# Kernel optimization log

Hardware: AMD Instinct MI355X
Metric: run time of the kernel (lower is better)

Reference implementation:

```python
import jax, jax.numpy as jnp
import numpy as np
from jax import lax

EDGES = [(11,12),(11,23),(12,24),(23,24),(23,25),(25,27),(24,26),(26,28),(11,13),(13,15),(12,14),(14,16)]
J = 33

def _build_neighbors():
    nb = [[j] for j in range(J)]
    for a, b in EDGES:
        nb[a].append(b); nb[b].append(a)
    K = max(len(n) for n in nb)
    idx = np.zeros((J, K), np.int32)
    msk = np.zeros((J, K), np.float32)
    for j, n in enumerate(nb):
        idx[j, :len(n)] = n; msk[j, :len(n)] = 1.0
    return jnp.asarray(idx), jnp.asarray(msk)

NBR_IDX, NBR_MASK = _build_neighbors()
BN_EPS = 1e-5

def conv(x, w, b):
    y = lax.conv_general_dilated(x, w, (1, 1), 'SAME', dimension_numbers=('NCHW', 'OIHW', 'NCHW'))
    return y + b[None, :, None, None]

def bn(x, g, b):
    # eval-mode BatchNorm with running_mean=0, running_var=1
    s = g / jnp.sqrt(1.0 + BN_EPS)
    return x * s[None, :, None, None] + b[None, :, None, None]

def maxpool2(x):
    return lax.reduce_window(x, -jnp.inf, lax.max, (1, 1, 2, 2), (1, 1, 2, 2), 'VALID')

def deconv2x2(x, w, b):
    # ConvTranspose2d(k=2, s=2): w is [Cin, Cout, 2, 2]
    y = jnp.einsum('bcij,codk->boidjk', x, w)
    B, O, H, _, W, _ = y.shape
    return y.reshape(B, O, 2 * H, 2 * W) + b[None, :, None, None]

def forward(x, conv1_w, conv1_b, bn1_g, bn1_b, conv2_w, conv2_b, bn2_g, bn2_b,
            conv3_w, conv3_b, bn3_g, bn3_b, conv4_w, conv4_b, bn4_g, bn4_b,
            dc1_w, dc1_b, dc2_w, dc2_b, head_w, head_b, proj_w, proj_b,
            msg_w, msg_b, gru_w_ih, gru_w_hh, gru_b_ih, gru_b_hh,
            refine_w, refine_b, vis_w1, vis_b1, vis_w2, vis_b2):
    relu = jax.nn.relu
    h = bn(relu(conv(x, conv1_w, conv1_b)), bn1_g, bn1_b)
    h = bn(relu(conv(h, conv2_w, conv2_b)), bn2_g, bn2_b)
    h = maxpool2(h)
    h = bn(relu(conv(h, conv3_w, conv3_b)), bn3_g, bn3_b)
    h = maxpool2(h)
    enc = bn(relu(conv(h, conv4_w, conv4_b)), bn4_g, bn4_b)  # [B,256,H/4,W/4]
    f = relu(deconv2x2(enc, dc1_w, dc1_b))
    feat_map = relu(deconv2x2(f, dc2_w, dc2_b))  # [B,64,H,W]
    init_hm = jax.nn.sigmoid(conv(feat_map, head_w, head_b))  # [B,J,H,W]
    B, Jn, H, W = init_hm.shape
    sm = jax.nn.softmax(init_hm.reshape(B, Jn, H * W) / 0.1, axis=-1).reshape(B, Jn, H, W)
    w_idx = jnp.linspace(0.0, 1.0, W)
    h_idx = jnp.linspace(0.0, 1.0, H)
    pred_x = (sm.sum(-2) * w_idx).sum(-1)  # [B,J] in [0,1]
    pred_y = (sm.sum(-1) * h_idx).sum(-1)
    # grid_sample bilinear, align_corners=True: grid=(2p-1) -> pixel coord p*(dim-1)
    ix = pred_x * (W - 1)
    iy = pred_y * (H - 1)
    x0 = jnp.clip(jnp.floor(ix), 0, W - 1)
    y0 = jnp.clip(jnp.floor(iy), 0, H - 1)
    wx = ix - x0
    wy = iy - y0
    x0i = x0.astype(jnp.int32); x1i = jnp.clip(x0i + 1, 0, W - 1)
    y0i = y0.astype(jnp.int32); y1i = jnp.clip(y0i + 1, 0, H - 1)
    fm = feat_map.transpose(0, 2, 3, 1)  # [B,H,W,C]
    bidx = jnp.arange(B)[:, None]
    v00 = fm[bidx, y0i, x0i]; v01 = fm[bidx, y0i, x1i]
    v10 = fm[bidx, y1i, x0i]; v11 = fm[bidx, y1i, x1i]
    wx = wx[..., None]; wy = wy[..., None]
    joint = (v00 * (1 - wx) * (1 - wy) + v01 * wx * (1 - wy)
             + v10 * (1 - wx) * wy + v11 * wx * wy)  # [B,J,64]
    joint_feats = joint @ proj_w.T + proj_b
    # SkeletonGNN (all joints read original joint_feats -> fully parallel)
    gathered = joint_feats[:, NBR_IDX, :]  # [B,J,K,D]
    lin = gathered @ msg_w.T + msg_b
    m = NBR_MASK[None, :, :, None]
    msgs = (lin * m).sum(2) / NBR_MASK.sum(1)[None, :, None]  # [B,J,D]
    gi = msgs @ gru_w_ih.T + gru_b_ih
    gh = joint_feats @ gru_w_hh.T + gru_b_hh
    D = joint_feats.shape[-1]
    ir, iz, inn = gi[..., :D], gi[..., D:2 * D], gi[..., 2 * D:]
    hr, hz, hn = gh[..., :D], gh[..., D:2 * D], gh[..., 2 * D:]
    r = jax.nn.sigmoid(ir + hr)
    z = jax.nn.sigmoid(iz + hz)
    n = jnp.tanh(inn + r * hn)
    refined_feats = (1 - z) * n + z * joint_feats
    refined_bias = refined_feats.mean(-1)[:, :, None, None]
    refined_hm = jax.nn.sigmoid(conv(init_hm, refine_w, refine_b) + refined_bias)
    # visibility head: adaptive avg pool to 4x4 (enc HW divisible by 4), eval dropout = identity
    eB, eC, eH, eW = enc.shape
    p = enc.reshape(eB, eC, 4, eH // 4, 4, eW // 4).mean((3, 5))  # [B,256,4,4]
    v = jax.nn.relu(p.reshape(eB, -1) @ vis_w1.T + vis_b1)
    vis_pred = jax.nn.sigmoid(v @ vis_w2.T + vis_b2)
    return refined_hm, vis_pred

def setup_inputs() -> dict:
    key = jax.random.key(0)
    ks = iter(jax.random.split(key, 64))
    def w(shape, s=0.05):
        return (jax.random.normal(next(ks), shape, dtype=jnp.float32) * s)
    inp = {
        'x': jax.random.normal(next(ks), (16, 3, 256, 256), dtype=jnp.float32),
        'conv1_w': w((32, 3, 3, 3)), 'conv1_b': w((32,)), 'bn1_g': jnp.ones((32,)), 'bn1_b': jnp.zeros((32,)),
        'conv2_w': w((64, 32, 3, 3)), 'conv2_b': w((64,)), 'bn2_g': jnp.ones((64,)), 'bn2_b': jnp.zeros((64,)),
        'conv3_w': w((128, 64, 3, 3)), 'conv3_b': w((128,)), 'bn3_g': jnp.ones((128,)), 'bn3_b': jnp.zeros((128,)),
        'conv4_w': w((256, 128, 3, 3)), 'conv4_b': w((256,)), 'bn4_g': jnp.ones((256,)), 'bn4_b': jnp.zeros((256,)),
        'dc1_w': w((256, 128, 2, 2)), 'dc1_b': w((128,)),
        'dc2_w': w((128, 64, 2, 2)), 'dc2_b': w((64,)),
        'head_w': w((33, 64, 1, 1)), 'head_b': w((33,)),
        'proj_w': w((64, 64)), 'proj_b': w((64,)),
        'msg_w': w((64, 64)), 'msg_b': w((64,)),
        'gru_w_ih': w((192, 64)), 'gru_w_hh': w((192, 64)),
        'gru_b_ih': w((192,)), 'gru_b_hh': w((192,)),
        'refine_w': w((33, 33, 3, 3)), 'refine_b': w((33,)),
        'vis_w1': w((256, 256 * 16)), 'vis_b1': w((256,)),
        'vis_w2': w((33, 256)), 'vis_b2': w((33,)),
    }
    return inp

def reference(x, conv1_w, conv1_b, bn1_g, bn1_b, conv2_w, conv2_b, bn2_g, bn2_b,
              conv3_w, conv3_b, bn3_g, bn3_b, conv4_w, conv4_b, bn4_g, bn4_b,
              dc1_w, dc1_b, dc2_w, dc2_b, head_w, head_b, proj_w, proj_b,
              msg_w, msg_b, gru_w_ih, gru_w_hh, gru_b_ih, gru_b_hh,
              refine_w, refine_b, vis_w1, vis_b1, vis_w2, vis_b2):
    return forward(x, conv1_w, conv1_b, bn1_g, bn1_b, conv2_w, conv2_b, bn2_g, bn2_b,
                   conv3_w, conv3_b, bn3_g, bn3_b, conv4_w, conv4_b, bn4_g, bn4_b,
                   dc1_w, dc1_b, dc2_w, dc2_b, head_w, head_b, proj_w, proj_b,
                   msg_w, msg_b, gru_w_ih, gru_w_hh, gru_b_ih, gru_b_hh,
                   refine_w, refine_b, vis_w1, vis_b1, vis_w2, vis_b2)
```

## Files before the change

### kernel.cpp

```cpp
#include <hip/hip_runtime.h>
#include <hip/hip_bf16.h>
#include <math.h>

#define BN_RS 0.99999500003749977f

typedef __attribute__((ext_vector_type(8))) __bf16 bf16x8;
typedef __attribute__((ext_vector_type(4))) float f32x4;

union U16 { uint4 u; bf16x8 v; __hip_bfloat16 h[8]; };
union U8  { uint2 u; __hip_bfloat16 h[4]; };

__device__ __forceinline__ float sigf(float v) { return 1.0f / (1.0f + expf(-v)); }

__global__ __launch_bounds__(256)
void repack_conv_w_k(const float* __restrict__ w, __hip_bfloat16* __restrict__ wb,
                     int taps, int Co, int Ci, int CoT, int Kp)
{
    int i = blockIdx.x * 256 + threadIdx.x;
    int tot = taps * CoT * Kp;
    if (i >= tot) return;
    int k = i % Kp, n = (i / Kp) % CoT, t = i / (Kp * CoT);
    float v = (n < Co && k < Ci) ? w[((long)n * Ci + k) * taps + t] : 0.0f;
    wb[i] = __float2bfloat16(v);
}
__global__ __launch_bounds__(256)
void repack_conv_w_ilv_k(const float* __restrict__ w, __hip_bfloat16* __restrict__ wb,
                         int taps, int Co, int Ci, int CoT, int Kp)
{
    int i = blockIdx.x * 256 + threadIdx.x;
    int tot = taps * CoT * Kp;
    if (i >= tot) return;
    int k = i % Kp, n = (i / Kp) % CoT, t = i / (Kp * CoT);
    int grp = n >> 6, r = n & 63;
    int c = (grp << 6) + (r & 15) * 4 + (r >> 4);
    float v = (c < Co && k < Ci) ? w[((long)c * Ci + k) * taps + t] : 0.0f;
    wb[i] = __float2bfloat16(v);
}
__global__ __launch_bounds__(256)
void repack_deconv_w_ilv_k(const float* __restrict__ w, __hip_bfloat16* __restrict__ wb,
                           int Co, int Ci)
{
    int i = blockIdx.x * 256 + threadIdx.x;
    int tot = 4 * Co * Ci;
    if (i >= tot) return;
    int k = i % Ci, n = (i / Ci) % Co, q = i / (Ci * Co);
    int grp = n >> 6, r = n & 63;
    int c = (grp << 6) + (r & 15) * 4 + (r >> 4);
    wb[i] = __float2bfloat16(w[((long)k * Co + c) * 4 + q]);
}

__global__ __launch_bounds__(256)
void zero_halo_k(__hip_bfloat16* __restrict__ buf, int H, int W, int C, int B)
{
    const int P = W + 2;
    const long per = (long)(2 * P + 2 * H) * C;
    long idx = (long)blockIdx.x * 256 + threadIdx.x;
    if (idx >= per * B) return;
    int b = (int)(idx / per);
    long r = idx % per;
    long off;
    if (r < (long)2 * P * C) {
        int row = (r >= (long)P * C) ? (H + 1) : 0;
        long r2 = r % ((long)P * C);
        off = (((long)b * (H + 2) + row) * P) * C + r2;
    } else {
        long r2 = r - (long)2 * P * C;
        int row = 1 + (int)(r2 / (2 * C));
        int side = (int)((r2 / C) & 1);
        int ch = (int)(r2 % C);
        off = (((long)b * (H + 2) + row) * P + (side ? (W + 1) : 0)) * C + ch;
    }
    buf[off] = __float2bfloat16(0.0f);
}

__global__ __launch_bounds__(256)
void conv1_k(const float* __restrict__ x, const float* __restrict__ w,
             const float* __restrict__ cb, const float* __restrict__ g,
             const float* __restrict__ bb, __hip_bfloat16* __restrict__ out)
{
    __shared__ float sw[216];
    const int tid = threadIdx.x;
    const int b = blockIdx.z >> 2, cg = blockIdx.z & 3, co0 = cg * 8;
    for (int i = tid; i < 216; i += 256) {
        int t = i % 9, co = (i / 9) % 8, ci = i / 72;
        sw[i] = w[((co0 + co) * 3 + ci) * 9 + t];
    }
    __syncthreads();
    const int tx = tid & 15, ty = tid >> 4;
    const int y = blockIdx.y * 16 + ty;
    const int xs = blockIdx.x * 64 + tx;
    float acc[4][8];
#pragma unroll
    for (int p = 0; p < 4; ++p)
#pragma unroll
        for (int c = 0; c < 8; ++c) acc[p][c] = 0.0f;
    for (int ci = 0; ci < 3; ++ci) {
        const float* plane = x + ((long)b * 3 + ci) * 65536;
#pragma unroll
        for (int t = 0; t < 9; ++t) {
            const int dy = t / 3 - 1, dx = t % 3 - 1;
            const int yy = y + dy;
            if ((unsigned)yy < 256u) {
                const float* row = plane + yy * 256;
                float wsr[8];
#pragma unroll
                for (int c = 0; c < 8; ++c) wsr[c] = sw[ci * 72 + c * 9 + t];
#pragma unroll
                for (int p = 0; p < 4; ++p) {
                    const int xx = xs + p * 16 + dx;
                    const float v = ((unsigned)xx < 256u) ? row[xx] : 0.0f;
#pragma unroll
                    for (int c = 0; c < 8; ++c) acc[p][c] = fmaf(v, wsr[c], acc[p][c]);
                }
            }
        }
    }
#pragma unroll
    for (int p = 0; p < 4; ++p) {
        U16 o;
#pragma unroll
        for (int c = 0; c < 8; ++c) {
            const int cc = co0 + c;
            float v = fmaxf(acc[p][c] + cb[cc], 0.0f) * (g[cc] * BN_RS) + bb[cc];
            o.h[c] = __float2bfloat16(v);
        }
        *(uint4*)(void*)(out + ((long)b * 2130048L + ((long)y * 258 + xs + p * 16) * 32) + co0) = o.u;
    }
}

template<int MI>
__global__ __launch_bounds__(256)
void mfma_conv_k(const __hip_bfloat16* __restrict__ in,
                 const __hip_bfloat16* __restrict__ wb,
                 const float* __restrict__ cbias,
                 const float* __restrict__ bng, const float* __restrict__ bnb,
                 __hip_bfloat16* __restrict__ out_bf,
                 int H, int W, int Cin, int PIT, long bstride, long obstride, int OPIT,
                 int CoutT, int CG, int S)
{
    const int tid = threadIdx.x;
    const int wid = tid >> 6, lane = tid & 63;
    const int ln = lane & 15, kg = lane >> 4;
    const int nx = gridDim.x;
    const int bx = (blockIdx.x & 7) * (nx >> 3) + (blockIdx.x >> 3);
    const int u = bx * 4 + wid;
    const int y = u / S, x0 = (u % S) * (MI * 16);
    const int b = blockIdx.z / CG, cg = blockIdx.z % CG;
    const int co0 = cg * 64;
    const int KC = Cin >> 5;

    f32x4 acc[MI][4];
#pragma unroll
    for (int i = 0; i < MI; ++i)
#pragma unroll
        for (int j = 0; j < 4; ++j) acc[i][j] = f32x4{0.f, 0.f, 0.f, 0.f};

    for (int kc = 0; kc < KC; ++kc) {
        const int kofs = kc * 32 + kg * 8;
#pragma unroll
        for (int t = 0; t < 9; ++t) {
            const int dy = t / 3 - 1, dx = t % 3 - 1;
            bf16x8 wfr[4];
#pragma unroll
            for (int ni = 0; ni < 4; ++ni)
                wfr[ni] = *(const bf16x8*)(const void*)(wb + ((long)t * CoutT + co0 + ni * 16 + ln) * Cin + kofs);
            U16 av[MI];
            const long rowb = (long)b * bstride + (long)(y + dy) * PIT * Cin + kofs;
#pragma unroll
            for (int mi = 0; mi < MI; ++mi)
                av[mi].u = *(const uint4*)(const void*)(in + rowb + (long)(x0 + mi * 16 + ln + dx) * Cin);
#pragma unroll
            for (int mi = 0; mi < MI; ++mi)
#pragma unroll
                for (int ni = 0; ni < 4; ++ni)
                    acc[mi][ni] = __builtin_amdgcn_mfma_f32_16x16x32_bf16(av[mi].v, wfr[ni], acc[mi][ni], 0, 0, 0);
        }
    }
#pragma unroll
    for (int mi = 0; mi < MI; ++mi) {
#pragma unroll
        for (int r = 0; r < 4; ++r) {
            const int px = x0 + mi * 16 + kg * 4 + r;
            const long pb = (long)b * obstride + ((long)y * OPIT + px) * CoutT + co0;
            U8 o;
#pragma unroll
            for (int ni = 0; ni < 4; ++ni) {
                const int c = co0 + ln * 4 + ni;
                float v = acc[mi][ni][r] + cbias[c];
                v = fmaxf(v, 0.0f) * (bng[c] * BN_RS) + bnb[c];
                o.h[ni] = __float2bfloat16(v);
            }
            *(uint2*)(void*)(out_bf + pb + ln * 4) = o.u;
        }
    }
}

__global__ __launch_bounds__(256)
void mfma_deconv_k(const __hip_bfloat16* __restrict__ in,
                   const __hip_bfloat16* __restrict__ wb,
                   const float* __restrict__ bias,
                   __hip_bfloat16* __restrict__ out,
                   int H, int W, int Cin, int CoutT, int CG, int S)
{
    const int tid = threadIdx.x;
    const int wid = tid >> 6, lane = tid & 63;
    const int ln = lane & 15, kg = lane >> 4;
    const int nx = gridDim.x;
    const int bx = (blockIdx.x & 7) * (nx >> 3) + (blockIdx.x >> 3);
    const int u = bx * 4 + wid;
    const int y = u / S, x0 = (u % S) * 32;
    const int b = blockIdx.z / CG, cg = blockIdx.z % CG;
    const int co0 = cg * 64;
    const int KC = Cin >> 5;
    const long inb = (long)b * H * W * Cin;
    const int W2 = W * 2;
    const long ob = (long)b * 4 * H * W * CoutT;

    for (int q = 0; q < 4; ++q) {
        const int dy = q >> 1, dx = q & 1;
        f32x4 acc[2][4];
#pragma unroll
        for (int i = 0; i < 2; ++i)
#pragma unroll
            for (int j = 0; j < 4; ++j) acc[i][j] = f32x4{0.f, 0.f, 0.f, 0.f};
        for (int kc = 0; kc < KC; ++kc) {
            const int kofs = kc * 32 + kg * 8;
            bf16x8 wfr[4];
            U16 av[2];
#pragma unroll
            for (int ni = 0; ni < 4; ++ni)
                wfr[ni] = *(const bf16x8*)(const void*)(wb + ((long)q * CoutT + co0 + ni * 16 + ln) * Cin + kofs);
#pragma unroll
            for (int mi = 0; mi < 2; ++mi)
                av[mi].u = *(const uint4*)(const void*)(in + inb + ((long)y * W + x0 + mi * 16 + ln) * Cin + kofs);
#pragma unroll
            for (int mi = 0; mi < 2; ++mi)
#pragma unroll
                for (int ni = 0; ni < 4; ++ni)
                    acc[mi][ni] = __builtin_amdgcn_mfma_f32_16x16x32_bf16(av[mi].v, wfr[ni], acc[mi][ni], 0, 0, 0);
        }
#pragma unroll
        for (int mi = 0; mi < 2; ++mi) {
#pragma unroll
            for (int r = 0; r < 4; ++r) {
                const int xl = x0 + mi * 16 + kg * 4 + r;
                const long pb = ob + ((long)(2 * y + dy) * W2 + 2 * xl + dx) * CoutT + co0;
                U8 o;
#pragma unroll
                for (int ni = 0; ni < 4; ++ni) {
                    const int c = co0 + ln * 4 + ni;
                    float v = fmaxf(acc[mi][ni][r] + bias[c], 0.0f);
                    o.h[ni] = __float2bfloat16(v);
                }
                *(uint2*)(void*)(out + pb + ln * 4) = o.u;
            }
        }
    }
}

template<int MODE>
__global__ __launch_bounds__(256)
void mfma_convT_k(const __hip_bfloat16* __restrict__ in,
                  const __hip_bfloat16* __restrict__ wb,
                  const float* __restrict__ cbias, const float* __restrict__ ebias,
                  __hip_bfloat16* __restrict__ out_bf, float* __restrict__ out_f32,
                  int H, int W, int Cin, int PIT, long bstride, long obstride, int OPIT,
                  int CoutT, int S)
{
    extern __shared__ float ltr[];
    const int tid = threadIdx.x;
    const int wid = tid >> 6, lane = tid & 63;
    const int ln = lane & 15, kg = lane >> 4;
    const int nx = gridDim.x;
    const int bx = (blockIdx.x & 7) * (nx >> 3) + (blockIdx.x >> 3);
    const int u = bx * 4 + wid;
    const int y = u / S, x0 = (u % S) * 32;
    const int b = blockIdx.z;
    const int KC = Cin >> 5;

    f32x4 acc[2][3];
#pragma unroll
    for (int i = 0; i < 2; ++i)
#pragma unroll
        for (int j = 0; j < 3; ++j) acc[i][j] = f32x4{0.f, 0.f, 0.f, 0.f};

    constexpr int NT = (MODE == 1) ? 1 : 9;
    for (int kc = 0; kc < KC; ++kc) {
        const int kofs = kc * 32 + kg * 8;
#pragma unroll
        for (int t = 0; t < NT; ++t) {
            const int dy = (MODE == 1) ? 0 : (t / 3 - 1);
            const int dx = (MODE == 1) ? 0 : (t % 3 - 1);
            bf16x8 wfr[3];
#pragma unroll
            for (int ni = 0; ni < 3; ++ni)
                wfr[ni] = *(const bf16x8*)(const void*)(wb + ((long)t * CoutT + ni * 16 + ln) * Cin + kofs);
            U16 av[2];
            const long rowb = (long)b * bstride + (long)(y + dy) * PIT * Cin + kofs;
#pragma unroll
            for (int mi = 0; mi < 2; ++mi)
                av[mi].u = *(const uint4*)(const void*)(in + rowb + (long)(x0 + mi * 16 + ln + dx) * Cin);
#pragma unroll
            for (int mi = 0; mi < 2; ++mi)
#pragma unroll
                for (int ni = 0; ni < 3; ++ni)
                    acc[mi][ni] = __builtin_amdgcn_mfma_f32_16x16x32_bf16(av[mi].v, wfr[ni], acc[mi][ni], 0, 0, 0);
        }
    }

    float* wt = ltr + wid * (48 * 35);
#pragma unroll
    for (int mi = 0; mi < 2; ++mi) {
#pragma unroll
        for (int r = 0; r < 4; ++r) {
            const int pxl = mi * 16 + kg * 4 + r;
            const int px = x0 + pxl;
#pragma unroll
            for (int ni = 0; ni < 3; ++ni) {
                const int c = ni * 16 + ln;
                float v = acc[mi][ni][r];
                if constexpr (MODE == 1) {
                    v = sigf(v + ((c < 33) ? cbias[c] : 0.0f));
                    out_bf[(long)b * obstride + ((long)y * OPIT + px) * CoutT + c] =
                        (c < 33) ? __float2bfloat16(v) : __float2bfloat16(0.0f);
                } else {
                    float eb = (c < 33) ? (cbias[c] + ebias[b * 33 + c]) : 0.0f;
                    v = sigf(v + eb);
                }
                wt[c * 35 + pxl] = v;
            }
        }
    }
    if (lane < 32) {
        const long o32 = ((long)b * 33) * H * W + (long)y * W + x0 + lane;
        for (int c = 0; c < 33; ++c)
            out_f32[o32 + (long)c * H * W] = wt[c * 35 + lane];
    }
}

__global__ __launch_bounds__(256)
void maxpool_bf_k(const __hip_bfloat16* __restrict__ in, __hip_bfloat16* __restrict__ out,
                  int Ho, int Wo, int C, long total, int OPIT, long obstride)
{
    long idx = (long)blockIdx.x * 256 + threadIdx.x;
    if (idx >= total) return;
    const int ng = C >> 3;
    const int cg = (int)(idx % ng);
    long pix = idx / ng;
    const int xo = (int)(pix % Wo); pix /= Wo;
    const int yo = (int)(pix % Ho);
    const int b = (int)(pix / Ho);
    const int Wi = Wo * 2;
    const __hip_bfloat16* p = in + (((long)b * 2 * Ho + 2 * yo) * Wi + 2 * xo) * C + cg * 8;
    U16 a0, a1, a2, a3, o;
    a0.u = *(const uint4*)(const void*)p;
    a1.u = *(const uint4*)(const void*)(p + C);
    a2.u = *(const uint4*)(const void*)(p + (long)Wi * C);
    a3.u = *(const uint4*)(const void*)(p + (long)Wi * C + C);
#pragma unroll
    for (int j = 0; j < 8; ++j) {
        float m = fmaxf(fmaxf(__bfloat162float(a0.h[j]), __bfloat162float(a1.h[j])),
                        fmaxf(__bfloat162float(a2.h[j]), __bfloat162float(a3.h[j])));
        o.h[j] = __float2bfloat16(m);
    }
    *(uint4*)(void*)(out + (long)b * obstride + ((long)yo * OPIT + xo) * C + cg * 8) = o.u;
}

__global__ __launch_bounds__(256)
void softargmax_k(const float* __restrict__ hm, float* __restrict__ coords)
{
    __shared__ float r0[256], r1[256], r2[256];
    const int bj = blockIdx.x;
    const int tid = threadIdx.x;
    const float* row = hm + (long)bj * 65536;
    float m = -1e30f;
    for (int i = tid; i < 65536; i += 256) m = fmaxf(m, row[i]);
    r0[tid] = m;
    __syncthreads();
    for (int s = 128; s > 0; s >>= 1) {
        if (tid < s) r0[tid] = fmaxf(r0[tid], r0[tid + s]);
        __syncthreads();
    }
    const float mx = r0[0];
    __syncthreads();
    float s = 0.0f, sx = 0.0f, sy = 0.0f;
    for (int i = tid; i < 65536; i += 256) {
        float e = expf((row[i] - mx) * 10.0f);
        s += e;
        sx += e * (float)(i & 255);
        sy += e * (float)(i >> 8);
    }
    r0[tid] = s; r1[tid] = sx; r2[tid] = sy;
    __syncthreads();
    for (int st = 128; st > 0; st >>= 1) {
        if (tid < st) { r0[tid] += r0[tid + st]; r1[tid] += r1[tid + st]; r2[tid] += r2[tid + st]; }
        __syncthreads();
    }
    if (tid == 0) {
        coords[2 * bj] = r1[0] / r0[0];
        coords[2 * bj + 1] = r2[0] / r0[0];
    }
}

__global__ __launch_bounds__(64)
void joint_bf_k(const __hip_bfloat16* __restrict__ fm, const float* __restrict__ coords,
                const float* __restrict__ pw, const float* __restrict__ pb,
                float* __restrict__ jf)
{
    __shared__ float sj[64];
    const int bj = blockIdx.x, b = bj / 33;
    const int tid = threadIdx.x;
    float ix = coords[2 * bj], iy = coords[2 * bj + 1];
    float x0f = fminf(fmaxf(floorf(ix), 0.0f), 255.0f);
    float y0f = fminf(fmaxf(floorf(iy), 0.0f), 255.0f);
    float wx = ix - x0f, wy = iy - y0f;
    int x0 = (int)x0f, y0 = (int)y0f;
    int x1 = min(x0 + 1, 255), y1 = min(y0 + 1, 255);
    const __hip_bfloat16* base = fm + (long)b * 65536 * 64 + tid;
    float v00 = __bfloat162float(base[((long)y0 * 256 + x0) * 64]);
    float v01 = __bfloat162float(base[((long)y0 * 256 + x1) * 64]);
    float v10 = __bfloat162float(base[((long)y1 * 256 + x0) * 64]);
    float v11 = __bfloat162float(base[((long)y1 * 256 + x1) * 64]);
    sj[tid] = v00 * (1 - wx) * (1 - wy) + v01 * wx * (1 - wy)
            + v10 * (1 - wx) * wy + v11 * wx * wy;
    __syncthreads();
    float a = pb[tid];
    for (int k = 0; k < 64; ++k) a = fmaf(sj[k], pw[tid * 64 + k], a);
    jf[(long)bj * 64 + tid] = a;
}

__device__ const int d_nbr[33][4] = {
    {0,0,0,0},{1,0,0,0},{2,0,0,0},{3,0,0,0},{4,0,0,0},{5,0,0,0},{6,0,0,0},{7,0,0,0},
    {8,0,0,0},{9,0,0,0},{10,0,0,0},
    {11,12,23,13},{12,11,24,14},{13,11,15,0},{14,12,16,0},{15,13,0,0},{16,14,0,0},
    {17,0,0,0},{18,0,0,0},{19,0,0,0},{20,0,0,0},{21,0,0,0},{22,0,0,0},
    {23,11,24,25},{24,12,23,26},{25,23,27,0},{26,24,28,0},{27,25,0,0},{28,26,0,0},
    {29,0,0,0},{30,0,0,0},{31,0,0,0},{32,0,0,0}};
__device__ const int d_cnt[33] = {1,1,1,1,1,1,1,1,1,1,1,4,4,3,3,2,2,1,1,1,1,1,1,4,4,3,3,2,2,1,1,1,1};

__global__ __launch_bounds__(192)
void gru_k(const float* __restrict__ jf, const float* __restrict__ mw, const float* __restrict__ mb,
           const float* __restrict__ wih, const float* __restrict__ whh,
           const float* __restrict__ bih, const float* __restrict__ bhh,
           float* __restrict__ rbias)
{
    __shared__ float s_mjf[64], s_jf[64], s_msg[64], s_gi[192], s_gh[192], s_ref[64];
    const int bj = blockIdx.x;
    const int b = bj / 33, j = bj % 33;
    const int tid = threadIdx.x;
    if (tid < 64) {
        int cnt = d_cnt[j];
        float s = 0.0f;
        for (int n = 0; n < 4; ++n)
            if (n < cnt) s += jf[((long)b * 33 + d_nbr[j][n]) * 64 + tid];
        s_mjf[tid] = s / (float)cnt;
        s_jf[tid] = jf[(long)bj * 64 + tid];
    }
    __syncthreads();
    if (tid < 64) {
        float a = mb[tid];
        for (int k = 0; k < 64; ++k) a = fmaf(mw[tid * 64 + k], s_mjf[k], a);
        s_msg[tid] = a;
    }
    __syncthreads();
    {
        float a = bih[tid], c = bhh[tid];
        for (int k = 0; k < 64; ++k) {
            a = fmaf(wih[tid * 64 + k], s_msg[k], a);
            c = fmaf(whh[tid * 64 + k], s_jf[k], c);
        }
        s_gi[tid] = a; s_gh[tid] = c;
    }
    __syncthreads();
    if (tid < 64) {
        float r = sigf(s_gi[tid] + s_gh[tid]);
        float z = sigf(s_gi[64 + tid] + s_gh[64 + tid]);
        float n = tanhf(s_gi[128 + tid] + r * s_gh[128 + tid]);
        s_ref[tid] = (1.0f - z) * n + z * s_jf[tid];
    }
    __syncthreads();
    if (tid == 0) {
        float s = 0.0f;
        for (int k = 0; k < 64; ++k) s += s_ref[k];
        rbias[bj] = s * (1.0f / 64.0f);
    }
}

__global__ __launch_bounds__(256)
void vispool_bf_k(const __hip_bfloat16* __restrict__ enc, float* __restrict__ p)
{
    int idx = blockIdx.x * 256 + threadIdx.x;
    int v = idx & 3, uu = (idx >> 2) & 3, c = (idx >> 4) & 255, b = idx >> 12;
    const __hip_bfloat16* base = enc + (long)b * 64 * 64 * 256 + c;
    float s = 0.0f;
    for (int a = 0; a < 16; ++a)
#pragma unroll
        for (int d = 0; d < 16; ++d)
            s += __bfloat162float(base[((long)(uu * 16 + a) * 64 + (v * 16 + d)) * 256]);
    p[idx] = s * (1.0f / 256.0f);
}

__global__ __launch_bounds__(256)
void visfc1_k(const float* __restrict__ p, const float* __restrict__ w1,
              const float* __restrict__ b1, float* __restrict__ v1)
{
    __shared__ float s_p[4096];
    const int b = blockIdx.x, tid = threadIdx.x;
    for (int i = tid; i < 4096; i += 256) s_p[i] = p[b * 4096 + i];
    __syncthreads();
    float a = b1[tid];
    const float* wr = w1 + (long)tid * 4096;
    for (int k = 0; k < 4096; ++k) a = fmaf(wr[k], s_p[k], a);
    v1[b * 256 + tid] = fmaxf(a, 0.0f);
}

__global__ __launch_bounds__(64)
void visfc2_k(const float* __restrict__ v1, const float* __restrict__ w2,
              const float* __restrict__ b2, float* __restrict__ out)
{
    const int b = blockIdx.x, t = threadIdx.x;
    if (t < 33) {
        float a = b2[t];
        for (int k = 0; k < 256; ++k) a = fmaf(w2[t * 256 + k], v1[b * 256 + k], a);
        out[b * 33 + t] = sigf(a);
    }
}

extern "C" void kernel_launch(void* const* d_in, const int* in_sizes, int n_in,
                              void* d_out, int out_size, void* d_ws, size_t ws_size,
                              hipStream_t stream)
{
    const float* x   = (const float*)d_in[0];
    const float* c1w = (const float*)d_in[1];  const float* c1b = (const float*)d_in[2];
    const float* b1g = (const float*)d_in[3];  const float* b1b = (const float*)d_in[4];
    const float* c2w = (const float*)d_in[5];  const float* c2b = (const float*)d_in[6];
    const float* b2g = (const float*)d_in[7];  const float* b2b = (const float*)d_in[8];
    const float* c3w = (const float*)d_in[9];  const float* c3b = (const float*)d_in[10];
    const float* b3g = (const float*)d_in[11]; const float* b3b = (const float*)d_in[12];
    const float* c4w = (const float*)d_in[13]; const float* c4b = (const float*)d_in[14];
    const float* b4g = (const float*)d_in[15]; const float* b4b = (const float*)d_in[16];
    const float* d1w = (const float*)d_in[17]; const float* d1b = (const float*)d_in[18];
    const float* d2w = (const float*)d_in[19]; const float* d2b = (const float*)d_in[20];
    const float* hw  = (const float*)d_in[21]; const float* hb  = (const float*)d_in[22];
    const float* pw  = (const float*)d_in[23]; const float* pb  = (const float*)d_in[24];
    const float* mw  = (const float*)d_in[25]; const float* mb  = (const float*)d_in[26];
    const float* wih = (const float*)d_in[27]; const float* whh = (const float*)d_in[28];
    const float* bih = (const float*)d_in[29]; const float* bhh = (const float*)d_in[30];
    const float* rw  = (const float*)d_in[31]; const float* rb  = (const float*)d_in[32];
    const float* v1w = (const float*)d_in[33]; const float* v1b = (const float*)d_in[34];
    const float* v2w = (const float*)d_in[35]; const float* v2b = (const float*)d_in[36];

    char* ws = (char*)d_ws;
    __hip_bfloat16* ENC  = (__hip_bfloat16*)(ws + 0L);
    __hip_bfloat16* R1   = (__hip_bfloat16*)(ws + 33554432L);
    __hip_bfloat16* R2   = (__hip_bfloat16*)(ws + 167772160L);
    char*           R3c  = ws + 304095232L;
    char* SM = ws + 442507264L;

    __hip_bfloat16* H1B = R1;                 __hip_bfloat16* H1I = R1 + 8288;
    __hip_bfloat16* P1B = R1;                 __hip_bfloat16* P1I = R1 + 8384;
    __hip_bfloat16* FEAT = R1;
    __hip_bfloat16* H3  = R2;
    __hip_bfloat16* F   = R2;
    __hip_bfloat16* HDB = R2;                 __hip_bfloat16* HDI = R2 + 16576;
    __hip_bfloat16* P2B = (__hip_bfloat16*)R3c; __hip_bfloat16* P2I = P2B + 8576;
    float*          INITHM = (float*)R3c;

    __hip_bfloat16* W2B = (__hip_bfloat16*)(SM + 0);
    __hip_bfloat16* W3B = (__hip_bfloat16*)(SM + 36864);
    __hip_bfloat16* W4B = (__hip_bfloat16*)(SM + 184320);
    __hip_bfloat16* WRB = (__hip_bfloat16*)(SM + 774144);
    __hip_bfloat16* WHB = (__hip_bfloat16*)(SM + 847872);
    __hip_bfloat16* WD1 = (__hip_bfloat16*)(SM + 856064);
    __hip_bfloat16* WD2 = (__hip_bfloat16*)(SM + 1118208);
    float* CO = (float*)(SM + 1183744);
    float* JF = (float*)(SM + 1187968);
    float* RB = (float*)(SM + 1323136);
    float* P  = (float*)(SM + 1325248);
    float* V1 = (float*)(SM + 1587392);

    float* out_hm  = (float*)d_out;
    float* out_vis = out_hm + 34603008L;
    __hip_bfloat16* H2 = (__hip_bfloat16*)d_out;

    repack_conv_w_ilv_k<<<(9*64*32 + 255)/256, 256, 0, stream>>>(c2w, W2B, 9, 64, 32, 64, 32);
    repack_conv_w_ilv_k<<<(9*128*64 + 255)/256, 256, 0, stream>>>(c3w, W3B, 9, 128, 64, 128, 64);
    repack_conv_w_ilv_k<<<(9*256*128 + 255)/256, 256, 0, stream>>>(c4w, W4B, 9, 256, 128, 256, 128);
    repack_conv_w_k<<<(9*64*64 + 255)/256, 256, 0, stream>>>(rw, WRB, 9, 33, 33, 64, 64);
    repack_conv_w_k<<<(1*64*64 + 255)/256, 256, 0, stream>>>(hw, WHB, 1, 33, 64, 64, 64);
    repack_deconv_w_ilv_k<<<(4*128*256 + 255)/256, 256, 0, stream>>>(d1w, WD1, 128, 256);
    repack_deconv_w_ilv_k<<<(4*64*128 + 255)/256, 256, 0, stream>>>(d2w, WD2, 64, 128);

    zero_halo_k<<<(526336 + 255)/256, 256, 0, stream>>>(H1B, 256, 256, 32, 16);
    zero_halo_k<<<(532480 + 255)/256, 256, 0, stream>>>(P2B, 64, 64, 128, 16);

    conv1_k<<<dim3(4, 16, 64), 256, 0, stream>>>(x, c1w, c1b, b1g, b1b, H1I);
    mfma_conv_k<2><<<dim3(512, 1, 16), 256, 0, stream>>>(
        H1I, W2B, c2b, b2g, b2b, H2,
        256, 256, 32, 258, 2130048L, 4194304L, 256, 64, 1, 8);
    zero_halo_k<<<(528384 + 255)/256, 256, 0, stream>>>(P1B, 128, 128, 64, 16);
    maxpool_bf_k<<<8192, 256, 0, stream>>>(H2, P1I, 128, 128, 64, 2097152L, 130, 1081600L);
    mfma_conv_k<2><<<dim3(128, 1, 32), 256, 0, stream>>>(
        P1I, W3B, c3b, b3g, b3b, H3,
        128, 128, 64, 130, 1081600L, 2097152L, 128, 128, 2, 4);
    maxpool_bf_k<<<4096, 256, 0, stream>>>(H3, P2I, 64, 64, 128, 1048576L, 66, 557568L);
    mfma_conv_k<2><<<dim3(32, 1, 64), 256, 0, stream>>>(
        P2I, W4B, c4b, b4g, b4b, ENC,
        64, 64, 128, 66, 557568L, 1048576L, 64, 256, 4, 2);
    mfma_deconv_k<<<dim3(32, 1, 32), 256, 0, stream>>>(
        ENC, WD1, d1b, F, 64, 64, 256, 128, 2, 2);
    mfma_deconv_k<<<dim3(128, 1, 16), 256, 0, stream>>>(
        F, WD2, d2b, FEAT, 128, 128, 128, 64, 1, 4);
    zero_halo_k<<<(1052672 + 255)/256, 256, 0, stream>>>(HDB, 256, 256, 64, 16);
    mfma_convT_k<1><<<dim3(512, 1, 16), 256, 26880, stream>>>(
        FEAT, WHB, hb, nullptr, HDI, INITHM,
        256, 256, 64, 256, 4194304L, 4260096L, 258, 64, 8);
    softargmax_k<<<528, 256, 0, stream>>>(INITHM, CO);
    joint_bf_k<<<528, 64, 0, stream>>>(FEAT, CO, pw, pb, JF);
    gru_k<<<528, 192, 0, stream>>>(JF, mw, mb, wih, whh, bih, bhh, RB);
    mfma_convT_k<2><<<dim3(512, 1, 16), 256, 26880, stream>>>(
        HDI, WRB, rb, RB, nullptr, out_hm,
        256, 256, 64, 258, 4260096L, 0L, 0, 64, 8);
    vispool_bf_k<<<256, 256, 0, stream>>>(ENC, P);
    visfc1_k<<<16, 256, 0, stream>>>(P, v1w, v1b, V1);
    visfc2_k<<<16, 64, 0, stream>>>(V1, v2w, v2b, out_vis);
}
```

Baseline: 1.731 ms.

## Drop fp32 init heatmap, softargmax from bf16 NHWC, coalesce refine stores

The head conv no longer writes a separate fp32 NCHW heatmap. It writes only the bf16 padded NHWC buffer with packed 4-channel stores, using interleaved weights. Softargmax now reads that bf16 NHWC buffer directly, handling 8 joints per block on a 16x5 grid instead of 528 blocks. The refine kernel's output is staged in shared memory and written cooperatively as 128-pixel contiguous runs per channel with rotated channel order, replacing 32-lane strided stores. The intent is to cut memory traffic and improve store coalescing. The tradeoffs are softargmax precision from bf16 inputs and far fewer softargmax blocks, which limits parallelism.

```diff
diff --git a/kernel.cpp b/kernel.cpp
--- a/kernel.cpp
+++ b/kernel.cpp
@@ -258,25 +258,76 @@
     }
 }
 
-template<int MODE>
-__global__ __launch_bounds__(256)
-void mfma_convT_k(const __hip_bfloat16* __restrict__ in,
-                  const __hip_bfloat16* __restrict__ wb,
-                  const float* __restrict__ cbias, const float* __restrict__ ebias,
-                  __hip_bfloat16* __restrict__ out_bf, float* __restrict__ out_f32,
-                  int H, int W, int Cin, int PIT, long bstride, long obstride, int OPIT,
-                  int CoutT, int S)
-{
-    extern __shared__ float ltr[];
+__global__ __launch_bounds__(256)
+void mfma_head_k(const __hip_bfloat16* __restrict__ in,
+                 const __hip_bfloat16* __restrict__ wb,
+                 const float* __restrict__ hb,
+                 __hip_bfloat16* __restrict__ out)
+{
     const int tid = threadIdx.x;
     const int wid = tid >> 6, lane = tid & 63;
     const int ln = lane & 15, kg = lane >> 4;
     const int nx = gridDim.x;
     const int bx = (blockIdx.x & 7) * (nx >> 3) + (blockIdx.x >> 3);
     const int u = bx * 4 + wid;
-    const int y = u / S, x0 = (u % S) * 32;
+    const int y = u >> 3, x0 = (u & 7) * 32;
     const int b = blockIdx.z;
-    const int KC = Cin >> 5;
+
+    f32x4 acc[2][4];
+#pragma unroll
+    for (int i = 0; i < 2; ++i)
+#pragma unroll
+        for (int j = 0; j < 4; ++j) acc[i][j] = f32x4{0.f, 0.f, 0.f, 0.f};
+
+    for (int kc = 0; kc < 2; ++kc) {
+        const int kofs = kc * 32 + kg * 8;
+        bf16x8 wfr[4];
+#pragma unroll
+        for (int ni = 0; ni < 4; ++ni)
+            wfr[ni] = *(const bf16x8*)(const void*)(wb + ((long)(ni * 16 + ln)) * 64 + kofs);
+        U16 av[2];
+#pragma unroll
+        for (int mi = 0; mi < 2; ++mi)
+            av[mi].u = *(const uint4*)(const void*)(in + (long)b * 4194304L + ((long)y * 256 + x0 + mi * 16 + ln) * 64 + kofs);
+#pragma unroll
+        for (int mi = 0; mi < 2; ++mi)
+#pragma unroll
+            for (int ni = 0; ni < 4; ++ni)
+                acc[mi][ni] = __builtin_amdgcn_mfma_f32_16x16x32_bf16(av[mi].v, wfr[ni], acc[mi][ni], 0, 0, 0);
+    }
+#pragma unroll
+    for (int mi = 0; mi < 2; ++mi) {
+#pragma unroll
+        for (int r = 0; r < 4; ++r) {
+            const int px = x0 + mi * 16 + kg * 4 + r;
+            const long pb = (long)b * 4260096L + ((long)y * 258 + px) * 64;
+            U8 o;
+#pragma unroll
+            for (int ni = 0; ni < 4; ++ni) {
+                const int c = ln * 4 + ni;
+                float v = (c < 33) ? sigf(acc[mi][ni][r] + hb[c]) : 0.0f;
+                o.h[ni] = __float2bfloat16(v);
+            }
+            *(uint2*)(void*)(out + pb + ln * 4) = o.u;
+        }
+    }
+}
+
+__global__ __launch_bounds__(256)
+void mfma_refine_k(const __hip_bfloat16* __restrict__ in,
+                   const __hip_bfloat16* __restrict__ wb,
+                   const float* __restrict__ cbias, const float* __restrict__ ebias,
+                   float* __restrict__ out_f32)
+{
+    extern __shared__ float ltr[];
+    const int tid = threadIdx.x;
+    const int wid = tid >> 6, lane = tid & 63;
+    const int ln = lane & 15, kg = lane >> 4;
+    const int nx = gridDim.x;
+    const int bx = (blockIdx.x & 7) * (nx >> 3) + (blockIdx.x >> 3);
+    const int u = bx * 4 + wid;
+    const int y = u >> 3, x0 = (u & 7) * 32;
+    const int b = blockIdx.z;
 
     f32x4 acc[2][3];
 #pragma unroll
@@ -284,22 +335,20 @@
 #pragma unroll
         for (int j = 0; j < 3; ++j) acc[i][j] = f32x4{0.f, 0.f, 0.f, 0.f};
 
-    constexpr int NT = (MODE == 1) ? 1 : 9;
-    for (int kc = 0; kc < KC; ++kc) {
+    for (int kc = 0; kc < 2; ++kc) {
         const int kofs = kc * 32 + kg * 8;
 #pragma unroll
-        for (int t = 0; t < NT; ++t) {
-            const int dy = (MODE == 1) ? 0 : (t / 3 - 1);
-            const int dx = (MODE == 1) ? 0 : (t % 3 - 1);
+        for (int t = 0; t < 9; ++t) {
+            const int dy = t / 3 - 1, dx = t % 3 - 1;
             bf16x8 wfr[3];
 #pragma unroll
             for (int ni = 0; ni < 3; ++ni)
-                wfr[ni] = *(const bf16x8*)(const void*)(wb + ((long)t * CoutT + ni * 16 + ln) * Cin + kofs);
+                wfr[ni] = *(const bf16x8*)(const void*)(wb + ((long)t * 64 + ni * 16 + ln) * 64 + kofs);
             U16 av[2];
-            const long rowb = (long)b * bstride + (long)(y + dy) * PIT * Cin + kofs;
+            const long rowb = (long)b * 4260096L + (long)(y + dy) * 258 * 64 + kofs;
 #pragma unroll
             for (int mi = 0; mi < 2; ++mi)
-                av[mi].u = *(const uint4*)(const void*)(in + rowb + (long)(x0 + mi * 16 + ln + dx) * Cin);
+                av[mi].u = *(const uint4*)(const void*)(in + rowb + (long)(x0 + mi * 16 + ln + dx) * 64);
 #pragma unroll
             for (int mi = 0; mi < 2; ++mi)
 #pragma unroll
@@ -308,33 +357,29 @@
         }
     }
 
-    float* wt = ltr + wid * (48 * 35);
+    float* wt = ltr + wid * 1680;
 #pragma unroll
     for (int mi = 0; mi < 2; ++mi) {
 #pragma unroll
         for (int r = 0; r < 4; ++r) {
             const int pxl = mi * 16 + kg * 4 + r;
-            const int px = x0 + pxl;
 #pragma unroll
             for (int ni = 0; ni < 3; ++ni) {
                 const int c = ni * 16 + ln;
-                float v = acc[mi][ni][r];
-                if constexpr (MODE == 1) {
-                    v = sigf(v + ((c < 33) ? cbias[c] : 0.0f));
-                    out_bf[(long)b * obstride + ((long)y * OPIT + px) * CoutT + c] =
-                        (c < 33) ? __float2bfloat16(v) : __float2bfloat16(0.0f);
-                } else {
-                    float eb = (c < 33) ? (cbias[c] + ebias[b * 33 + c]) : 0.0f;
-                    v = sigf(v + eb);
-                }
-                wt[c * 35 + pxl] = v;
+                float eb = (c < 33) ? (cbias[c] + ebias[b * 33 + c]) : 0.0f;
+                wt[c * 35 + pxl] = sigf(acc[mi][ni][r] + eb);
             }
         }
     }
-    if (lane < 32) {
-        const long o32 = ((long)b * 33) * H * W + (long)y * W + x0 + lane;
-        for (int c = 0; c < 33; ++c)
-            out_f32[o32 + (long)c * H * W] = wt[c * 35 + lane];
+    __syncthreads();
+    const int yb = (bx * 4) >> 3;
+    const int xb = ((bx * 4) & 7) * 32;
+    const int coff = bx % 33;
+    for (int i = tid; i < 4224; i += 256) {
+        int cl = i >> 7, p = i & 127;
+        int c = cl + coff; if (c >= 33) c -= 33;
+        float v = ltr[(p >> 5) * 1680 + c * 35 + (p & 31)];
+        out_f32[((long)b * 33 + c) * 65536L + (long)yb * 256 + xb + p] = v;
     }
 }
 
@@ -367,38 +412,68 @@
 }
 
 __global__ __launch_bounds__(256)
-void softargmax_k(const float* __restrict__ hm, float* __restrict__ coords)
-{
-    __shared__ float r0[256], r1[256], r2[256];
-    const int bj = blockIdx.x;
-    const int tid = threadIdx.x;
-    const float* row = hm + (long)bj * 65536;
-    float m = -1e30f;
-    for (int i = tid; i < 65536; i += 256) m = fmaxf(m, row[i]);
-    r0[tid] = m;
+void softargmax_nhwc_k(const __hip_bfloat16* __restrict__ hd, float* __restrict__ coords)
+{
+    __shared__ float sm[8][256];
+    __shared__ float fin[8][4];
+    const int b = blockIdx.x, jg = blockIdx.y;
+    const int tid = threadIdx.x;
+    const __hip_bfloat16* base = hd + (long)b * 4260096L + jg * 8;
+    float m[8];
+#pragma unroll
+    for (int c = 0; c < 8; ++c) m[c] = -1e30f;
+    for (int i = tid; i < 65536; i += 256) {
+        int y = i >> 8, x = i & 255;
+        U16 v; v.u = *(const uint4*)(const void*)(base + ((long)y * 258 + x) * 64);
+#pragma unroll
+        for (int c = 0; c < 8; ++c) m[c] = fmaxf(m[c], __bfloat162float(v.h[c]));
+    }
+#pragma unroll
+    for (int c = 0; c < 8; ++c) sm[c][tid] = m[c];
     __syncthreads();
     for (int s = 128; s > 0; s >>= 1) {
-        if (tid < s) r0[tid] = fmaxf(r0[tid], r0[tid + s]);
+        if (tid < s)
+#pragma unroll
+            for (int c = 0; c < 8; ++c) sm[c][tid] = fmaxf(sm[c][tid], sm[c][tid + s]);
         __syncthreads();
     }
-    const float mx = r0[0];
-    __syncthreads();
-    float s = 0.0f, sx = 0.0f, sy = 0.0f;
+    if (tid < 8) fin[tid][0] = sm[tid][0];
+    __syncthreads();
+#pragma unroll
+    for (int c = 0; c < 8; ++c) m[c] = fin[c][0];
+    float s8[8], sx8[8], sy8[8];
+#pragma unroll
+    for (int c = 0; c < 8; ++c) { s8[c] = 0.f; sx8[c] = 0.f; sy8[c] = 0.f; }
     for (int i = tid; i < 65536; i += 256) {
-        float e = expf((row[i] - mx) * 10.0f);
-        s += e;
-        sx += e * (float)(i & 255);
-        sy += e * (float)(i >> 8);
-    }
-    r0[tid] = s; r1[tid] = sx; r2[tid] = sy;
-    __syncthreads();
-    for (int st = 128; st > 0; st >>= 1) {
-        if (tid < st) { r0[tid] += r0[tid + st]; r1[tid] += r1[tid + st]; r2[tid] += r2[tid + st]; }
+        int y = i >> 8, x = i & 255;
+        U16 v; v.u = *(const uint4*)(const void*)(base + ((long)y * 258 + x) * 64);
+#pragma unroll
+        for (int c = 0; c < 8; ++c) {
+            float e = expf((__bfloat162float(v.h[c]) - m[c]) * 10.0f);
+            s8[c] += e; sx8[c] += e * (float)x; sy8[c] += e * (float)y;
+        }
+    }
+    for (int which = 0; which < 3; ++which) {
         __syncthreads();
-    }
-    if (tid == 0) {
-        coords[2 * bj] = r1[0] / r0[0];
-        coords[2 * bj + 1] = r2[0] / r0[0];
+#pragma unroll
+        for (int c = 0; c < 8; ++c)
+            sm[c][tid] = (which == 0) ? s8[c] : (which == 1) ? sx8[c] : sy8[c];
+        __syncthreads();
+        for (int s = 128; s > 0; s >>= 1) {
+            if (tid < s)
+#pragma unroll
+                for (int c = 0; c < 8; ++c) sm[c][tid] += sm[c][tid + s];
+            __syncthreads();
+        }
+        if (tid < 8) fin[tid][1 + which] = sm[tid][0];
+    }
+    __syncthreads();
+    if (tid < 8) {
+        int j = jg * 8 + tid;
+        if (j < 33) {
+            coords[2 * (b * 33 + j)]     = fin[tid][2] / fin[tid][1];
+            coords[2 * (b * 33 + j) + 1] = fin[tid][3] / fin[tid][1];
+        }
     }
 }
 
@@ -564,7 +639,6 @@
     __hip_bfloat16* F   = R2;
     __hip_bfloat16* HDB = R2;                 __hip_bfloat16* HDI = R2 + 16576;
     __hip_bfloat16* P2B = (__hip_bfloat16*)R3c; __hip_bfloat16* P2I = P2B + 8576;
-    float*          INITHM = (float*)R3c;
 
     __hip_bfloat16* W2B = (__hip_bfloat16*)(SM + 0);
     __hip_bfloat16* W3B = (__hip_bfloat16*)(SM + 36864);
@@ -587,7 +661,7 @@
     repack_conv_w_ilv_k<<<(9*128*64 + 255)/256, 256, 0, stream>>>(c3w, W3B, 9, 128, 64, 128, 64);
     repack_conv_w_ilv_k<<<(9*256*128 + 255)/256, 256, 0, stream>>>(c4w, W4B, 9, 256, 128, 256, 128);
     repack_conv_w_k<<<(9*64*64 + 255)/256, 256, 0, stream>>>(rw, WRB, 9, 33, 33, 64, 64);
-    repack_conv_w_k<<<(1*64*64 + 255)/256, 256, 0, stream>>>(hw, WHB, 1, 33, 64, 64, 64);
+    repack_conv_w_ilv_k<<<(1*64*64 + 255)/256, 256, 0, stream>>>(hw, WHB, 1, 33, 64, 64, 64);
     repack_deconv_w_ilv_k<<<(4*128*256 + 255)/256, 256, 0, stream>>>(d1w, WD1, 128, 256);
     repack_deconv_w_ilv_k<<<(4*64*128 + 255)/256, 256, 0, stream>>>(d2w, WD2, 64, 128);
 
@@ -612,15 +686,12 @@
     mfma_deconv_k<<<dim3(128, 1, 16), 256, 0, stream>>>(
         F, WD2, d2b, FEAT, 128, 128, 128, 64, 1, 4);
     zero_halo_k<<<(1052672 + 255)/256, 256, 0, stream>>>(HDB, 256, 256, 64, 16);
-    mfma_convT_k<1><<<dim3(512, 1, 16), 256, 26880, stream>>>(
-        FEAT, WHB, hb, nullptr, HDI, INITHM,
-        256, 256, 64, 256, 4194304L, 4260096L, 258, 64, 8);
-    softargmax_k<<<528, 256, 0, stream>>>(INITHM, CO);
+    mfma_head_k<<<dim3(512, 1, 16), 256, 0, stream>>>(FEAT, WHB, hb, HDI);
+    softargmax_nhwc_k<<<dim3(16, 5), 256, 0, stream>>>(HDI, CO);
     joint_bf_k<<<528, 64, 0, stream>>>(FEAT, CO, pw, pb, JF);
     gru_k<<<528, 192, 0, stream>>>(JF, mw, mb, wih, whh, bih, bhh, RB);
-    mfma_convT_k<2><<<dim3(512, 1, 16), 256, 26880, stream>>>(
-        HDI, WRB, rb, RB, nullptr, out_hm,
-        256, 256, 64, 258, 4260096L, 0L, 0, 64, 8);
+    mfma_refine_k<<<dim3(512, 1, 16), 256, 26880, stream>>>(
+        HDI, WRB, rb, RB, out_hm);
     vispool_bf_k<<<256, 256, 0, stream>>>(ENC, P);
     visfc1_k<<<16, 256, 0, stream>>>(P, v1w, v1b, V1);
     visfc2_k<<<16, 64, 0, stream>>>(V1, v2w, v2b, out_vis);
```

Result: slower. 1.856 ms (+7.2%).
